# Kernel tuning notes

Hardware: AMD Instinct MI355X
Metric: run time of the kernel (lower is better)

## Reference

```python
import jax, jax.numpy as jnp
import numpy as np

B, S, V, E, H, K = 64, 512, 50000, 128, 256, 20
PAD_IDX, SOS_IDX = 0, 19
NEG = -9999.0


def _lstm_dir(x, mask, W_ih, W_hh, b):
    # x: [B,S,E], mask: [B,S] float. PyTorch gate order: i,f,g,o.
    xg = jnp.einsum('bse,ge->bsg', x, W_ih) + b  # [B,S,4H]

    def step(carry, inp):
        h, c = carry
        xg_t, m = inp  # [B,4H], [B,1]
        g = xg_t + h @ W_hh.T
        i, f, gg, o = jnp.split(g, 4, axis=-1)
        i = jax.nn.sigmoid(i); f = jax.nn.sigmoid(f); o = jax.nn.sigmoid(o)
        gg = jnp.tanh(gg)
        c_new = f * c + i * gg
        h_new = o * jnp.tanh(c_new)
        h = m * h_new + (1.0 - m) * h
        c = m * c_new + (1.0 - m) * c
        return (h, c), h * m  # packed/pad_packed => zeros at padding

    h0 = jnp.zeros((x.shape[0], W_hh.shape[1]), x.dtype)
    _, hs = jax.lax.scan(step, (h0, h0), (xg.transpose(1, 0, 2), mask.T[:, :, None]))
    return hs.transpose(1, 0, 2)  # [B,S,H]


def setup_inputs() -> dict:
    key = jax.random.key(0)
    ks = jax.random.split(key, 12)
    word_seq = jax.random.randint(ks[0], (B, S), 0, V)
    tags = jax.random.randint(ks[1], (B, S), 1, K - 1)  # avoid pad(0) and sos(K-1)
    lengths = S // 2 + jax.random.randint(ks[2], (B,), 0, S // 2)
    sc = 0.1
    embed = jax.random.normal(ks[3], (V, E), jnp.float32) * sc
    W_ih_f = jax.random.normal(ks[4], (4 * H, E), jnp.float32) * sc
    W_hh_f = jax.random.normal(ks[5], (4 * H, H), jnp.float32) * sc
    b_f = jnp.zeros((4 * H,), jnp.float32).at[H:2 * H].set(1.0)  # forget bias 1
    W_ih_b = jax.random.normal(ks[6], (4 * H, E), jnp.float32) * sc
    W_hh_b = jax.random.normal(ks[7], (4 * H, H), jnp.float32) * sc
    b_b = jnp.zeros((4 * H,), jnp.float32).at[H:2 * H].set(1.0)
    lin_W = jax.random.normal(ks[8], (K, 2 * H), jnp.float32) * sc
    lin_b = jnp.zeros((K,), jnp.float32)
    trans = jax.random.normal(ks[9], (K, K), jnp.float32) * 0.1 - 1.0
    trans = trans.at[SOS_IDX, :].set(NEG).at[:, PAD_IDX].set(NEG)
    trans = trans.at[PAD_IDX, :].set(NEG).at[PAD_IDX, PAD_IDX].set(0.0)
    return dict(word_seq=word_seq, tags=tags, lengths=lengths, embed=embed,
                W_ih_f=W_ih_f, W_hh_f=W_hh_f, b_f=b_f,
                W_ih_b=W_ih_b, W_hh_b=W_hh_b, b_b=b_b,
                lin_W=lin_W, lin_b=lin_b, trans=trans)


def reference(word_seq, tags, lengths, embed, W_ih_f, W_hh_f, b_f,
              W_ih_b, W_hh_b, b_b, lin_W, lin_b, trans):
    mask = (jnp.arange(S)[None, :] < lengths[:, None]).astype(jnp.float32)  # [B,S]
    x = embed[word_seq]  # [B,S,E]

    # forward direction
    h_f = _lstm_dir(x, mask, W_ih_f, W_hh_f, b_f)
    # backward direction: reverse within each valid length (packed-seq semantics)
    t = jnp.arange(S)[None, :]
    ri = jnp.where(t < lengths[:, None], lengths[:, None] - 1 - t, t)  # [B,S]
    x_rev = jnp.take_along_axis(x, ri[:, :, None], axis=1)
    h_b_rev = _lstm_dir(x_rev, mask, W_ih_b, W_hh_b, b_b)
    h_b = jnp.take_along_axis(h_b_rev, ri[:, :, None], axis=1)

    rnn_out = jnp.concatenate([h_f, h_b], axis=-1)  # [B,S,2H]
    feats = jnp.einsum('bsd,kd->bsk', rnn_out, lin_W) + lin_b  # [B,S,K]

    # --- CRF numerator: score of gold path ---
    states = jnp.concatenate(
        [jnp.full((B, 1), SOS_IDX, dtype=tags.dtype), tags], axis=1)  # [B,S+1]
    emis = jnp.take_along_axis(feats, tags[:, :, None], axis=-1)[..., 0]  # [B,S]
    trn = trans[states[:, 1:], states[:, :-1]]  # [B,S]
    numerator = jnp.sum((emis + trn) * mask, axis=1)  # [B]

    # --- CRF denominator: forward algorithm (log partition) ---
    score0 = jnp.full((B, K), NEG, jnp.float32).at[:, SOS_IDX].set(0.0)

    def step(score, inp):
        em, m = inp  # [B,K], [B,1]
        new = jax.nn.logsumexp(
            score[:, None, :] + em[:, :, None] + trans[None, :, :], axis=-1)
        score = m * new + (1.0 - m) * score
        return score, None

    score, _ = jax.lax.scan(
        step, score0, (feats.transpose(1, 0, 2), mask.T[:, :, None]))
    denominator = jax.nn.logsumexp(score, axis=-1)  # [B]

    return denominator - numerator  # per-example negative log-likelihood [B]
```

## Files before the change

kernel.cpp:

```cpp
#include <hip/hip_runtime.h>
#include <hip/hip_fp16.h>
#include <stdint.h>

#define BB 64
#define SS 512
#define EE 128
#define HH 256
#define KK 20
#define NEGV -9999.0f
#define SOS_IDX 19

typedef unsigned int u32;

__device__ __forceinline__ float sigm(float x){ return 1.0f / (1.0f + __expf(-x)); }
__device__ __forceinline__ float tanh_fast(float x){
  float e = __expf(2.f * x);
  return 1.f - 2.f / (e + 1.f);
}

__device__ __forceinline__ void pk4(uint4 w, const __half2* hp,
                                    __half2& a0, __half2& a1, __half2& a2, __half2& a3){
  __half2 w0 = *(__half2*)&w.x, w1 = *(__half2*)&w.y, w2 = *(__half2*)&w.z, w3 = *(__half2*)&w.w;
  a0 = __hfma2(w0, hp[0], a0);
  a1 = __hfma2(w1, hp[1], a1);
  a2 = __hfma2(w2, hp[2], a2);
  a3 = __hfma2(w3, hp[3], a3);
}
__device__ __forceinline__ float flushacc(__half2& a0, __half2& a1, __half2& a2, __half2& a3){
  float2 f0 = __half22float2(a0), f1 = __half22float2(a1);
  float2 f2 = __half22float2(a2), f3 = __half22float2(a3);
  __half2 z = __floats2half2_rn(0.f, 0.f);
  a0 = z; a1 = z; a2 = z; a3 = z;
  return ((f0.x + f0.y) + (f1.x + f1.y)) + ((f2.x + f2.y) + (f3.x + f3.y));
}

__global__ void prep_whh(const float* __restrict__ whh_f, const float* __restrict__ whh_b,
                         __half* __restrict__ wp){
  int id = blockIdx.x * 256 + threadIdx.x;
  if (id >= 524288) return;
  int d = id >> 18;
  int rem = id & 262143;
  int row = rem >> 8;
  int k = rem & 255;
  const float* w = d ? whh_b : whh_f;
  wp[(((size_t)d * 32 + (k >> 3)) * 1024 + row) * 8 + (k & 7)] = __float2half(w[row * 256 + k]);
}

__global__ void prep_wih(const float* __restrict__ wih_f, const float* __restrict__ wih_b,
                         float* __restrict__ wt){
  int id = blockIdx.x * 256 + threadIdx.x;
  if (id >= 262144) return;
  int d = id >> 17;
  int rem = id & 131071;
  int col = rem >> 7;
  int k = rem & 127;
  const float* w = d ? wih_b : wih_f;
  wt[(size_t)k * 2048 + d * 1024 + col] = w[col * 128 + k];
}

__global__ __launch_bounds__(256) void xg_gemm(const int* __restrict__ word_seq,
    const float* __restrict__ embed, const float* __restrict__ wt,
    const float* __restrict__ b_f, const float* __restrict__ b_b,
    __half* __restrict__ xg){
  __shared__ __align__(16) float xs[16][128];
  int rb = blockIdx.x >> 1, cb = blockIdx.x & 1;
  int tid = threadIdx.x;
  {
    int r = tid >> 4, kq = (tid & 15) * 8;
    int bs = rb * 16 + r;
    int w = word_seq[bs];
    const float* er = embed + (size_t)w * 128 + kq;
    float4 a = *(const float4*)er;
    float4 b = *(const float4*)(er + 4);
    *(float4*)&xs[r][kq] = a;
    *(float4*)&xs[r][kq + 4] = b;
  }
  __syncthreads();
  int co = tid * 4;
  const float* bias = cb ? b_b : b_f;
  float4 bv = *(const float4*)(bias + co);
  float4 acc[16];
  #pragma unroll
  for (int r = 0; r < 16; r++) acc[r] = bv;
  const float* wptr = wt + cb * 1024 + co;
  for (int k = 0; k < 128; k++){
    float4 w4 = *(const float4*)(wptr + (size_t)k * 2048);
    #pragma unroll
    for (int r = 0; r < 16; r++){
      float xv = xs[r][k];
      acc[r].x += xv * w4.x; acc[r].y += xv * w4.y;
      acc[r].z += xv * w4.z; acc[r].w += xv * w4.w;
    }
  }
  __half* base = xg + (size_t)cb * ((size_t)BB * SS * 1024);
  #pragma unroll
  for (int r = 0; r < 16; r++){
    int bs = rb * 16 + r;
    __half* o = base + (size_t)bs * 1024 + co;
    __half2 p0 = __floats2half2_rn(acc[r].x, acc[r].y);
    __half2 p1 = __floats2half2_rn(acc[r].z, acc[r].w);
    uint2 st; st.x = *(u32*)&p0; st.y = *(u32*)&p1;
    *(uint2*)o = st;
  }
}

__global__ __launch_bounds__(1024) void lstm_seq(const int* __restrict__ lengths,
    const __half* __restrict__ wp, const __half* __restrict__ xg,
    float* __restrict__ rnn){
  extern __shared__ __align__(16) char smem[];
  u32*     wl  = (u32*)smem;
  float*   gl  = (float*)(smem + 147456);
  __half2* hl2 = (__half2*)(smem + 151552);
  __half*  hlh = (__half*)(smem + 151552);

  int bx = blockIdx.x;
  int b = bx & 63, d = bx >> 6;
  int tid = threadIdx.x;
  int l = lengths[b];
  const uint4* wp4 = (const uint4*)(wp + (size_t)d * (32 * 1024 * 8));

  uint4 wr[6];
  #pragma unroll
  for (int c = 0; c < 6; c++) wr[c] = wp4[c * 1024 + tid];
  #pragma unroll
  for (int c = 0; c < 9; c++){
    uint4 v = wp4[(6 + c) * 1024 + tid];
    *(uint4*)&wl[(c * 1024 + tid) * 4] = v;
  }
  if (tid < 256) hlh[tid] = __float2half(0.f);
  float cc = 0.f;
  const __half* xgd = xg + ((size_t)d * BB * SS + (size_t)b * SS) * 1024;
  float* rbp = rnn + (size_t)b * SS * 512 + d * 256;
  for (int i = tid; i < (SS - l) * 256; i += 1024){
    int s = l + (i >> 8), j = i & 255;
    rbp[(size_t)s * 512 + j] = 0.f;
  }
  int gate = tid >> 8;
  const uint4* sp4 = wp4 + 15 * 1024;
  __syncthreads();

  for (int t = 0; t < l; t++){
    int s = d ? (l - 1 - t) : t;
    float xv = __half2float(xgd[(size_t)s * 1024 + tid]);
    uint4 s0[5];
    #pragma unroll
    for (int c = 0; c < 5; c++) s0[c] = sp4[c * 1024 + tid];

    __half2 z = __floats2half2_rn(0.f, 0.f);
    __half2 a0 = z, a1 = z, a2 = z, a3 = z;
    float fa;
    #pragma unroll
    for (int c = 0; c < 6; c++) pk4(wr[c], hl2 + c * 4, a0, a1, a2, a3);
    fa = flushacc(a0, a1, a2, a3);
    uint4 s1[5];
    #pragma unroll
    for (int c = 0; c < 5; c++) s1[c] = sp4[(5 + c) * 1024 + tid];
    #pragma unroll
    for (int c = 0; c < 9; c++){
      uint4 wv = *(const uint4*)&wl[(c * 1024 + tid) * 4];
      pk4(wv, hl2 + 24 + c * 4, a0, a1, a2, a3);
    }
    fa += flushacc(a0, a1, a2, a3);
    #pragma unroll
    for (int c = 0; c < 5; c++) pk4(s0[c], hl2 + 60 + c * 4, a0, a1, a2, a3);
    #pragma unroll
    for (int c = 0; c < 5; c++) s0[c] = sp4[(10 + c) * 1024 + tid];
    #pragma unroll
    for (int c = 0; c < 5; c++) pk4(s1[c], hl2 + 80 + c * 4, a0, a1, a2, a3);
    s1[0] = sp4[15 * 1024 + tid];
    s1[1] = sp4[16 * 1024 + tid];
    fa += flushacc(a0, a1, a2, a3);
    #pragma unroll
    for (int c = 0; c < 5; c++) pk4(s0[c], hl2 + 100 + c * 4, a0, a1, a2, a3);
    pk4(s1[0], hl2 + 120, a0, a1, a2, a3);
    pk4(s1[1], hl2 + 124, a0, a1, a2, a3);
    fa += flushacc(a0, a1, a2, a3);

    float a = fa + xv;
    float gv = (gate == 2) ? tanh_fast(a) : sigm(a);
    gl[tid] = gv;
    __syncthreads();
    if (tid < 256){
      float iv = gl[tid], fv = gl[tid + 256], gg = gl[tid + 512], ov = gl[tid + 768];
      cc = fv * cc + iv * gg;
      float h = ov * tanh_fast(cc);
      hlh[tid] = __float2half(h);
      rbp[(size_t)s * 512 + tid] = h;
    }
    __syncthreads();
  }
}

__global__ void feat_gemv(const float* __restrict__ rnn,
    const float* __restrict__ linW, const float* __restrict__ linb,
    float* __restrict__ feats){
  int id = blockIdx.x * 256 + threadIdx.x;
  if (id >= BB * SS * KK) return;
  int row = id / 20;
  int col = id - row * 20;
  const float* rr = rnn + (size_t)row * 512;
  const float* wr = linW + col * 512;
  float acc = linb[col];
  for (int k8 = 0; k8 < 64; k8++){
    float4 ra = *(const float4*)(rr + k8 * 8);
    float4 rb = *(const float4*)(rr + k8 * 8 + 4);
    float4 wa = *(const float4*)(wr + k8 * 8);
    float4 wb = *(const float4*)(wr + k8 * 8 + 4);
    acc += ra.x * wa.x + ra.y * wa.y + ra.z * wa.z + ra.w * wa.w
         + rb.x * wb.x + rb.y * wb.y + rb.z * wb.z + rb.w * wb.w;
  }
  feats[id] = acc;
}

__global__ __launch_bounds__(64) void crf_kernel(const int* __restrict__ tags,
    const int* __restrict__ lengths, const float* __restrict__ trans,
    const float* __restrict__ feats, float* __restrict__ out){
  int b = blockIdx.x, tid = threadIdx.x;
  __shared__ float tr[400];
  __shared__ float sc[20];
  for (int i = tid; i < 400; i += 64) tr[i] = trans[i];
  __syncthreads();
  int l = lengths[b];
  const int* tg = tags + b * SS;
  const float* fb = feats + (size_t)b * SS * 20;
  float p = 0.f;
  for (int s = tid; s < SS; s += 64){
    if (s < l){
      int cur = tg[s];
      int prev = s ? tg[s - 1] : SOS_IDX;
      p += fb[s * 20 + cur] + tr[cur * 20 + prev];
    }
  }
  #pragma unroll
  for (int off = 32; off; off >>= 1) p += __shfl_down(p, off);
  if (tid < 20) sc[tid] = (tid == SOS_IDX) ? 0.f : NEGV;
  __syncthreads();
  float em = (tid < 20 && l > 0) ? fb[tid] : 0.f;
  for (int s = 0; s < l; s++){
    float em_nxt = (tid < 20 && (s + 1) < l) ? fb[(s + 1) * 20 + tid] : 0.f;
    float nv = 0.f;
    if (tid < 20){
      const float* trow = &tr[tid * 20];
      float v[20];
      float m = -1e30f;
      #pragma unroll
      for (int jj = 0; jj < 20; jj++){ v[jj] = sc[jj] + trow[jj]; m = fmaxf(m, v[jj]); }
      float ssum = 0.f;
      #pragma unroll
      for (int jj = 0; jj < 20; jj++) ssum += __expf(v[jj] - m);
      nv = em + m + __logf(ssum);
    }
    __syncthreads();
    if (tid < 20) sc[tid] = nv;
    __syncthreads();
    em = em_nxt;
  }
  if (tid == 0){
    float m = -1e30f;
    #pragma unroll
    for (int i = 0; i < 20; i++) m = fmaxf(m, sc[i]);
    float ssum = 0.f;
    #pragma unroll
    for (int i = 0; i < 20; i++) ssum += __expf(sc[i] - m);
    out[b] = (m + __logf(ssum)) - p;
  }
}

extern "C" void kernel_launch(void* const* d_in, const int* in_sizes, int n_in,
                              void* d_out, int out_size, void* d_ws, size_t ws_size,
                              hipStream_t stream){
  const int*   word_seq = (const int*)d_in[0];
  const int*   tags     = (const int*)d_in[1];
  const int*   lengths  = (const int*)d_in[2];
  const float* embed    = (const float*)d_in[3];
  const float* wih_f    = (const float*)d_in[4];
  const float* whh_f    = (const float*)d_in[5];
  const float* b_f      = (const float*)d_in[6];
  const float* wih_b    = (const float*)d_in[7];
  const float* whh_b    = (const float*)d_in[8];
  const float* b_b      = (const float*)d_in[9];
  const float* linW     = (const float*)d_in[10];
  const float* linb     = (const float*)d_in[11];
  const float* trans    = (const float*)d_in[12];
  float* out = (float*)d_out;

  char* ws = (char*)d_ws;
  __half* wp    = (__half*)ws;
  float*  wt    = (float*)(ws + (1ull << 20));
  __half* xg    = (__half*)(ws + (2ull << 20));
  float*  rnn   = (float*)(ws + (2ull << 20) + (128ull << 20));
  float*  feats = (float*)(ws + (2ull << 20) + (192ull << 20));

  (void)hipFuncSetAttribute((const void*)lstm_seq,
        hipFuncAttributeMaxDynamicSharedMemorySize, 152064);

  prep_whh<<<dim3(2048), dim3(256), 0, stream>>>(whh_f, whh_b, wp);
  prep_wih<<<dim3(1024), dim3(256), 0, stream>>>(wih_f, wih_b, wt);
  xg_gemm<<<dim3(4096), dim3(256), 0, stream>>>(word_seq, embed, wt, b_f, b_b, xg);
  lstm_seq<<<dim3(128), dim3(1024), 152064, stream>>>(lengths, wp, xg, rnn);
  feat_gemv<<<dim3(2560), dim3(256), 0, stream>>>(rnn, linW, linb, feats);
  crf_kernel<<<dim3(64), dim3(64), 0, stream>>>(tags, lengths, trans, feats, out);
}
```

Baseline: 1.776 ms.

## Rebalance LSTM weight residency, double-buffer h, half rnn output, skip padded work

The recurrent kernel now keeps 18 weight chunks in registers, 9 in LDS and streams only 5 from global memory per step. It double-buffers the hidden state so all 1024 threads compute the cell update redundantly, and it stores rnn output in fp16. The xg GEMM and feature GEMV skip padded timesteps, and the CRF loop drops its __syncthreads since only lanes of one wavefront are active. The aim is to cut per-step global weight traffic and barrier cost, with the risk of register spills from the larger register tile, unzeroed padded rnn rows, and changed fp16 precision.

```diff
diff --git a/kernel.cpp b/kernel.cpp
--- a/kernel.cpp
+++ b/kernel.cpp
@@ -9,6 +9,10 @@
 #define KK 20
 #define NEGV -9999.0f
 #define SOS_IDX 19
+
+#define VC 18
+#define LC 9
+#define SC 5
 
 typedef unsigned int u32;
 
@@ -59,11 +63,16 @@
 }
 
 __global__ __launch_bounds__(256) void xg_gemm(const int* __restrict__ word_seq,
+    const int* __restrict__ lengths,
     const float* __restrict__ embed, const float* __restrict__ wt,
     const float* __restrict__ b_f, const float* __restrict__ b_b,
     __half* __restrict__ xg){
   __shared__ __align__(16) float xs[16][128];
   int rb = blockIdx.x >> 1, cb = blockIdx.x & 1;
+  {
+    int s0 = (rb * 16) & 511, bq = (rb * 16) >> 9;
+    if (s0 >= lengths[bq]) return;
+  }
   int tid = threadIdx.x;
   {
     int r = tid >> 4, kq = (tid & 15) * 8;
@@ -104,110 +113,107 @@
   }
 }
 
-__global__ __launch_bounds__(1024) void lstm_seq(const int* __restrict__ lengths,
+__global__ __launch_bounds__(1024, 4) void lstm_seq(const int* __restrict__ lengths,
     const __half* __restrict__ wp, const __half* __restrict__ xg,
-    float* __restrict__ rnn){
+    __half* __restrict__ rnn){
   extern __shared__ __align__(16) char smem[];
-  u32*     wl  = (u32*)smem;
-  float*   gl  = (float*)(smem + 147456);
-  __half2* hl2 = (__half2*)(smem + 151552);
-  __half*  hlh = (__half*)(smem + 151552);
+  u32*    wl = (u32*)smem;
+  float*  gl = (float*)(smem + 147456);
+  __half* hb = (__half*)(smem + 151552);
 
   int bx = blockIdx.x;
   int b = bx & 63, d = bx >> 6;
   int tid = threadIdx.x;
+  int u = tid & 255, g = tid >> 8;
   int l = lengths[b];
   const uint4* wp4 = (const uint4*)(wp + (size_t)d * (32 * 1024 * 8));
 
-  uint4 wr[6];
-  #pragma unroll
-  for (int c = 0; c < 6; c++) wr[c] = wp4[c * 1024 + tid];
-  #pragma unroll
-  for (int c = 0; c < 9; c++){
-    uint4 v = wp4[(6 + c) * 1024 + tid];
-    *(uint4*)&wl[(c * 1024 + tid) * 4] = v;
-  }
-  if (tid < 256) hlh[tid] = __float2half(0.f);
+  uint4 w[VC];
+  #pragma unroll
+  for (int c = 0; c < VC; c++) w[c] = wp4[c * 1024 + tid];
+  #pragma unroll
+  for (int c = 0; c < LC; c++)
+    *(uint4*)&wl[(c * 1024 + tid) * 4] = wp4[(VC + c) * 1024 + tid];
+  if (tid < 256) hb[tid] = __float2half(0.f);
   float cc = 0.f;
   const __half* xgd = xg + ((size_t)d * BB * SS + (size_t)b * SS) * 1024;
-  float* rbp = rnn + (size_t)b * SS * 512 + d * 256;
-  for (int i = tid; i < (SS - l) * 256; i += 1024){
-    int s = l + (i >> 8), j = i & 255;
-    rbp[(size_t)s * 512 + j] = 0.f;
-  }
-  int gate = tid >> 8;
-  const uint4* sp4 = wp4 + 15 * 1024;
+  __half* rbp = rnn + (size_t)b * SS * 512 + d * 256;
+  int cur = 0;
   __syncthreads();
 
   for (int t = 0; t < l; t++){
     int s = d ? (l - 1 - t) : t;
     float xv = __half2float(xgd[(size_t)s * 1024 + tid]);
-    uint4 s0[5];
-    #pragma unroll
-    for (int c = 0; c < 5; c++) s0[c] = sp4[c * 1024 + tid];
-
+    uint4 sw[SC];
+    #pragma unroll
+    for (int c = 0; c < SC; c++) sw[c] = wp4[(VC + LC + c) * 1024 + tid];
+
+    const __half* hc = &hb[cur * 256];
     __half2 z = __floats2half2_rn(0.f, 0.f);
     __half2 a0 = z, a1 = z, a2 = z, a3 = z;
     float fa;
     #pragma unroll
-    for (int c = 0; c < 6; c++) pk4(wr[c], hl2 + c * 4, a0, a1, a2, a3);
+    for (int c = 0; c < 16; c++){
+      uint4 hv = *(const uint4*)&hc[c * 8];
+      pk4(w[c], (const __half2*)&hv, a0, a1, a2, a3);
+    }
     fa = flushacc(a0, a1, a2, a3);
-    uint4 s1[5];
-    #pragma unroll
-    for (int c = 0; c < 5; c++) s1[c] = sp4[(5 + c) * 1024 + tid];
-    #pragma unroll
-    for (int c = 0; c < 9; c++){
+    #pragma unroll
+    for (int c = 16; c < VC; c++){
+      uint4 hv = *(const uint4*)&hc[c * 8];
+      pk4(w[c], (const __half2*)&hv, a0, a1, a2, a3);
+    }
+    #pragma unroll
+    for (int c = 0; c < LC; c++){
+      uint4 hv = *(const uint4*)&hc[(VC + c) * 8];
       uint4 wv = *(const uint4*)&wl[(c * 1024 + tid) * 4];
-      pk4(wv, hl2 + 24 + c * 4, a0, a1, a2, a3);
+      pk4(wv, (const __half2*)&hv, a0, a1, a2, a3);
+    }
+    #pragma unroll
+    for (int c = 0; c < SC; c++){
+      uint4 hv = *(const uint4*)&hc[(VC + LC + c) * 8];
+      pk4(sw[c], (const __half2*)&hv, a0, a1, a2, a3);
     }
     fa += flushacc(a0, a1, a2, a3);
-    #pragma unroll
-    for (int c = 0; c < 5; c++) pk4(s0[c], hl2 + 60 + c * 4, a0, a1, a2, a3);
-    #pragma unroll
-    for (int c = 0; c < 5; c++) s0[c] = sp4[(10 + c) * 1024 + tid];
-    #pragma unroll
-    for (int c = 0; c < 5; c++) pk4(s1[c], hl2 + 80 + c * 4, a0, a1, a2, a3);
-    s1[0] = sp4[15 * 1024 + tid];
-    s1[1] = sp4[16 * 1024 + tid];
-    fa += flushacc(a0, a1, a2, a3);
-    #pragma unroll
-    for (int c = 0; c < 5; c++) pk4(s0[c], hl2 + 100 + c * 4, a0, a1, a2, a3);
-    pk4(s1[0], hl2 + 120, a0, a1, a2, a3);
-    pk4(s1[1], hl2 + 124, a0, a1, a2, a3);
-    fa += flushacc(a0, a1, a2, a3);
-
-    float a = fa + xv;
-    float gv = (gate == 2) ? tanh_fast(a) : sigm(a);
+    fa += xv;
+
+    float gv = (g == 2) ? tanh_fast(fa) : sigm(fa);
     gl[tid] = gv;
     __syncthreads();
-    if (tid < 256){
-      float iv = gl[tid], fv = gl[tid + 256], gg = gl[tid + 512], ov = gl[tid + 768];
-      cc = fv * cc + iv * gg;
-      float h = ov * tanh_fast(cc);
-      hlh[tid] = __float2half(h);
-      rbp[(size_t)s * 512 + tid] = h;
-    }
+    float iv = gl[u], fv = gl[u + 256], ggv = gl[u + 512], ov = gl[u + 768];
+    cc = fv * cc + iv * ggv;
+    float h = ov * tanh_fast(cc);
+    if (g == 0)      hb[(cur ^ 1) * 256 + u] = __float2half(h);
+    else if (g == 1) rbp[(size_t)s * 512 + u] = __float2half(h);
     __syncthreads();
-  }
-}
-
-__global__ void feat_gemv(const float* __restrict__ rnn,
+    cur ^= 1;
+  }
+}
+
+__global__ void feat_gemv(const int* __restrict__ lengths,
+    const __half* __restrict__ rnn,
     const float* __restrict__ linW, const float* __restrict__ linb,
     float* __restrict__ feats){
   int id = blockIdx.x * 256 + threadIdx.x;
   if (id >= BB * SS * KK) return;
   int row = id / 20;
   int col = id - row * 20;
-  const float* rr = rnn + (size_t)row * 512;
+  int s = row & 511, bq = row >> 9;
+  if (s >= lengths[bq]) return;
+  const __half* rr = rnn + (size_t)row * 512;
   const float* wr = linW + col * 512;
   float acc = linb[col];
   for (int k8 = 0; k8 < 64; k8++){
-    float4 ra = *(const float4*)(rr + k8 * 8);
-    float4 rb = *(const float4*)(rr + k8 * 8 + 4);
+    uint4 rv = *(const uint4*)(rr + k8 * 8);
+    const __half2* h2 = (const __half2*)&rv;
+    float2 p0 = __half22float2(h2[0]);
+    float2 p1 = __half22float2(h2[1]);
+    float2 p2 = __half22float2(h2[2]);
+    float2 p3 = __half22float2(h2[3]);
     float4 wa = *(const float4*)(wr + k8 * 8);
     float4 wb = *(const float4*)(wr + k8 * 8 + 4);
-    acc += ra.x * wa.x + ra.y * wa.y + ra.z * wa.z + ra.w * wa.w
-         + rb.x * wb.x + rb.y * wb.y + rb.z * wb.z + rb.w * wb.w;
+    acc += p0.x * wa.x + p0.y * wa.y + p1.x * wa.z + p1.y * wa.w
+         + p2.x * wb.x + p2.y * wb.y + p3.x * wb.z + p3.y * wb.w;
   }
   feats[id] = acc;
 }
@@ -234,11 +240,9 @@
   #pragma unroll
   for (int off = 32; off; off >>= 1) p += __shfl_down(p, off);
   if (tid < 20) sc[tid] = (tid == SOS_IDX) ? 0.f : NEGV;
-  __syncthreads();
   float em = (tid < 20 && l > 0) ? fb[tid] : 0.f;
   for (int s = 0; s < l; s++){
     float em_nxt = (tid < 20 && (s + 1) < l) ? fb[(s + 1) * 20 + tid] : 0.f;
-    float nv = 0.f;
     if (tid < 20){
       const float* trow = &tr[tid * 20];
       float v[20];
@@ -248,11 +252,8 @@
       float ssum = 0.f;
       #pragma unroll
       for (int jj = 0; jj < 20; jj++) ssum += __expf(v[jj] - m);
-      nv = em + m + __logf(ssum);
-    }
-    __syncthreads();
-    if (tid < 20) sc[tid] = nv;
-    __syncthreads();
+      sc[tid] = em + m + __logf(ssum);
+    }
     em = em_nxt;
   }
   if (tid == 0){
@@ -288,16 +289,16 @@
   __half* wp    = (__half*)ws;
   float*  wt    = (float*)(ws + (1ull << 20));
   __half* xg    = (__half*)(ws + (2ull << 20));
-  float*  rnn   = (float*)(ws + (2ull << 20) + (128ull << 20));
-  float*  feats = (float*)(ws + (2ull << 20) + (192ull << 20));
+  __half* rnn   = (__half*)(ws + (2ull << 20) + (128ull << 20));
+  float*  feats = (float*)(ws + (2ull << 20) + (160ull << 20));
 
   (void)hipFuncSetAttribute((const void*)lstm_seq,
-        hipFuncAttributeMaxDynamicSharedMemorySize, 152064);
+        hipFuncAttributeMaxDynamicSharedMemorySize, 152576);
 
   prep_whh<<<dim3(2048), dim3(256), 0, stream>>>(whh_f, whh_b, wp);
   prep_wih<<<dim3(1024), dim3(256), 0, stream>>>(wih_f, wih_b, wt);
-  xg_gemm<<<dim3(4096), dim3(256), 0, stream>>>(word_seq, embed, wt, b_f, b_b, xg);
-  lstm_seq<<<dim3(128), dim3(1024), 152064, stream>>>(lengths, wp, xg, rnn);
-  feat_gemv<<<dim3(2560), dim3(256), 0, stream>>>(rnn, linW, linb, feats);
+  xg_gemm<<<dim3(4096), dim3(256), 0, stream>>>(word_seq, lengths, embed, wt, b_f, b_b, xg);
+  lstm_seq<<<dim3(128), dim3(1024), 152576, stream>>>(lengths, wp, xg, rnn);
+  feat_gemv<<<dim3(2560), dim3(256), 0, stream>>>(lengths, rnn, linW, linb, feats);
   crf_kernel<<<dim3(64), dim3(64), 0, stream>>>(tags, lengths, trans, feats, out);
 }
```

Measured after the change: 1.690 ms. 1.05x faster.
